# Kernel optimization log

Hardware: AMD Instinct MI355X
Metric: run time of the kernel (lower is better)

Reference implementation:

```python
import jax, jax.numpy as jnp
import numpy as np

GROUPS = 4

def shuffle(t):
    # torch Shuffle: transpose(-1,-2).contiguous().view(original_shape)
    return jnp.swapaxes(t, -1, -2).reshape(t.shape)

def setup_inputs() -> dict:
    key = jax.random.key(0)
    B, H = 131072, 512
    gh = 2 * H // GROUPS  # 256
    k = jax.random.split(key, 5)
    s = lambda fan_in: 1.0 / np.sqrt(fan_in)
    x = jax.random.normal(k[0], (B, H), dtype=jnp.float32)
    # weights stored as (in, out); Linear has bias=False throughout
    W1 = jax.random.uniform(k[1], (H, H), jnp.float32, -s(H), s(H))
    W2 = jax.random.uniform(k[2], (gh, gh), jnp.float32, -s(gh), s(gh))
    W3 = jax.random.uniform(k[3], (gh, gh), jnp.float32, -s(gh), s(gh))
    W4 = jax.random.uniform(k[4], (2 * H, H), jnp.float32, -s(2 * H), s(2 * H))
    return {"x": x, "W1": W1, "W2": W2, "W3": W3, "W4": W4}

def reference(x, W1, W2, W3, W4):
    B, H = x.shape
    gh = 2 * H // GROUPS
    sorted_x = jnp.sort(x, axis=1, stable=True)
    h = jnp.stack((x, sorted_x), axis=1)          # (B, 2, H)
    h = h @ W1                                    # (B, 2, H)
    h = h.reshape(B, GROUPS, gh)                  # Flatten + Unflatten
    h = shuffle(h)
    h = h @ W2                                    # (B, GROUPS, gh)
    h = shuffle(h)
    h = jax.nn.relu(h @ W3)                       # (B, GROUPS, gh)
    h = h.reshape(B, GROUPS * gh)                 # (B, 2H)
    scores = jax.nn.sigmoid(h @ W4)               # (B, H)
    return x * scores
```

## Files before the change

kernel.cpp:

```cpp
#include <hip/hip_runtime.h>
#include <hip/hip_bf16.h>
#include <cstdint>
#include <cstddef>

typedef short bf16x8 __attribute__((ext_vector_type(8)));
typedef float f32x4 __attribute__((ext_vector_type(4)));

#define BM 128
#define BN 128
#define BK 32

__device__ __forceinline__ void gl_lds16(const __hip_bfloat16* gp, __hip_bfloat16* lp) {
  __builtin_amdgcn_global_load_lds((const __attribute__((address_space(1))) void*)gp,
                                   (__attribute__((address_space(3))) void*)lp, 16, 0, 0);
}

__global__ void __launch_bounds__(256) wtrans_kernel(const float* __restrict__ src,
                                                     __hip_bfloat16* __restrict__ dst,
                                                     int R, int C) {
  int idx = blockIdx.x * 256 + threadIdx.x;
  if (idx >= R * C) return;
  int r = idx / C, c = idx % C;
  dst[(size_t)c * R + r] = __float2bfloat16(src[idx]);
}

__global__ void __launch_bounds__(256) sort_kernel(const float* __restrict__ x,
                                                   __hip_bfloat16* __restrict__ h0) {
  int row = blockIdx.x * 4 + (threadIdx.x >> 6);
  int lane = threadIdx.x & 63;
  const float* xr = x + (size_t)row * 512;

  float v[8];
  *(float4*)&v[0] = *(const float4*)&xr[lane * 8];
  *(float4*)&v[4] = *(const float4*)&xr[lane * 8 + 4];

  __hip_bfloat16* h = h0 + (size_t)row * 1024;
  {
    alignas(16) __hip_bfloat16 ob[8];
#pragma unroll
    for (int i = 0; i < 8; ++i) ob[i] = __float2bfloat16(v[i]);
    *(bf16x8*)&h[lane * 8] = *(const bf16x8*)ob;
  }

#pragma unroll
  for (int k = 2; k <= 512; k <<= 1) {
#pragma unroll
    for (int j = k >> 1; j > 0; j >>= 1) {
      if (j >= 8) {
        int L = j >> 3;
        bool lower = (lane & L) == 0;
        bool up = (((lane * 8) & k) == 0);
        bool sel = (lower == up);
#pragma unroll
        for (int r = 0; r < 8; ++r) {
          float pv = __shfl_xor(v[r], L, 64);
          float mn = fminf(v[r], pv), mx = fmaxf(v[r], pv);
          v[r] = sel ? mn : mx;
        }
      } else {
#pragma unroll
        for (int r = 0; r < 8; ++r) {
          if ((r & j) == 0) {
            int r2 = r | j;
            bool up = ((((lane * 8) + r) & k) == 0);
            float a = v[r], b = v[r2];
            float mn = fminf(a, b), mx = fmaxf(a, b);
            v[r] = up ? mn : mx;
            v[r2] = up ? mx : mn;
          }
        }
      }
    }
  }

  {
    alignas(16) __hip_bfloat16 ob[8];
#pragma unroll
    for (int i = 0; i < 8; ++i) ob[i] = __float2bfloat16(v[i]);
    *(bf16x8*)&h[512 + lane * 8] = *(const bf16x8*)ob;
  }
}

template <int EPI>
__global__ void __launch_bounds__(256) gemm_k(const __hip_bfloat16* __restrict__ A,
                                              const __hip_bfloat16* __restrict__ BT,
                                              __hip_bfloat16* __restrict__ Cb,
                                              float* __restrict__ Co,
                                              const float* __restrict__ X,
                                              int M, int N, int K) {
  __shared__ __hip_bfloat16 lA[BM * BK];
  __shared__ __hip_bfloat16 lB[BN * BK];

  int nwg = gridDim.x;
  int bid = blockIdx.x;
  int cpx = nwg >> 3;
  int wg = (bid & 7) * cpx + (bid >> 3);

  int nt = N / BN;
  int m0 = (wg / nt) * BM;
  int n0 = (wg % nt) * BN;

  int tid = threadIdx.x;
  int lane = tid & 63;
  int w = tid >> 6;
  int wm = (w >> 1) << 6;
  int wn = (w & 1) << 6;
  int r16 = lane & 15;
  int k8 = (lane >> 4) << 3;

  int colA = (lane & 3) * 8;
  int rsub = lane >> 2;
  int row0 = w * 16 + rsub;
  int row1 = (4 + w) * 16 + rsub;

  f32x4 acc[4][4] = {};

  for (int k0 = 0; k0 < K; k0 += BK) {
    gl_lds16(&A[(size_t)(m0 + row0) * K + k0 + colA], &lA[(size_t)w * 512]);
    gl_lds16(&A[(size_t)(m0 + row1) * K + k0 + colA], &lA[(size_t)(4 + w) * 512]);
    gl_lds16(&BT[(size_t)(n0 + row0) * K + k0 + colA], &lB[(size_t)w * 512]);
    gl_lds16(&BT[(size_t)(n0 + row1) * K + k0 + colA], &lB[(size_t)(4 + w) * 512]);
    asm volatile("s_waitcnt vmcnt(0)" ::: "memory");
    __syncthreads();

    bf16x8 af[4], bfr[4];
#pragma unroll
    for (int i = 0; i < 4; ++i)
      af[i] = *(const bf16x8*)&lA[(wm + 16 * i + r16) * BK + k8];
#pragma unroll
    for (int j = 0; j < 4; ++j)
      bfr[j] = *(const bf16x8*)&lB[(wn + 16 * j + r16) * BK + k8];
#pragma unroll
    for (int i = 0; i < 4; ++i)
#pragma unroll
      for (int j = 0; j < 4; ++j)
        acc[i][j] = __builtin_amdgcn_mfma_f32_16x16x32_bf16(af[i], bfr[j], acc[i][j], 0, 0, 0);
    __syncthreads();
  }

#pragma unroll
  for (int i = 0; i < 4; ++i) {
    int grow_base = m0 + wm + 16 * i + ((lane >> 4) << 2);
#pragma unroll
    for (int j = 0; j < 4; ++j) {
      int gcol = n0 + wn + 16 * j + (lane & 15);
#pragma unroll
      for (int r = 0; r < 4; ++r) {
        int grow = grow_base + r;
        float v = acc[i][j][r];
        if constexpr (EPI == 1) {
          int b = grow >> 1, p = grow & 1;
          Cb[(size_t)b * 1024 + 4 * (gcol & 255) + (p << 1) + (gcol >> 8)] = __float2bfloat16(v);
        } else if constexpr (EPI == 2) {
          int b = grow >> 2, g = grow & 3;
          Cb[(size_t)b * 1024 + 4 * gcol + g] = __float2bfloat16(v);
        } else if constexpr (EPI == 3) {
          Cb[(size_t)grow * N + gcol] = __float2bfloat16(fmaxf(v, 0.f));
        } else {
          float xv = X[(size_t)grow * N + gcol];
          Co[(size_t)grow * N + gcol] = xv / (1.f + __expf(-v));
        }
      }
    }
  }
}

extern "C" void kernel_launch(void* const* d_in, const int* in_sizes, int n_in,
                              void* d_out, int out_size, void* d_ws, size_t ws_size,
                              hipStream_t stream) {
  const float* x  = (const float*)d_in[0];
  const float* W1 = (const float*)d_in[1];
  const float* W2 = (const float*)d_in[2];
  const float* W3 = (const float*)d_in[3];
  const float* W4 = (const float*)d_in[4];

  const int B = 131072;

  char* ws = (char*)d_ws;
  __hip_bfloat16* W1T = (__hip_bfloat16*)(ws);
  __hip_bfloat16* W2T = (__hip_bfloat16*)(ws + 524288);
  __hip_bfloat16* W3T = (__hip_bfloat16*)(ws + 655360);
  __hip_bfloat16* W4T = (__hip_bfloat16*)(ws + 786432);
  __hip_bfloat16* bufA = (__hip_bfloat16*)(ws + 2097152);
  __hip_bfloat16* bufB = bufA + (size_t)134217728;

  wtrans_kernel<<<(512 * 512) / 256, 256, 0, stream>>>(W1, W1T, 512, 512);
  wtrans_kernel<<<(256 * 256) / 256, 256, 0, stream>>>(W2, W2T, 256, 256);
  wtrans_kernel<<<(256 * 256) / 256, 256, 0, stream>>>(W3, W3T, 256, 256);
  wtrans_kernel<<<(1024 * 512) / 256, 256, 0, stream>>>(W4, W4T, 1024, 512);

  sort_kernel<<<B / 4, 256, 0, stream>>>(x, bufA);

  gemm_k<1><<<(2 * B / BM) * (512 / BN), 256, 0, stream>>>(bufA, W1T, bufB, nullptr, nullptr,
                                                           2 * B, 512, 512);
  gemm_k<2><<<(4 * B / BM) * (256 / BN), 256, 0, stream>>>(bufB, W2T, bufA, nullptr, nullptr,
                                                           4 * B, 256, 256);
  gemm_k<3><<<(4 * B / BM) * (256 / BN), 256, 0, stream>>>(bufA, W3T, bufB, nullptr, nullptr,
                                                           4 * B, 256, 256);
  gemm_k<4><<<(B / BM) * (512 / BN), 256, 0, stream>>>(bufB, W4T, nullptr, (float*)d_out, x,
                                                       B, 512, 1024);
}
```

Measured before the change: 1.145 ms.

## Triple-buffer LDS tiles in GEMM to overlap global loads with MFMA

Replaces the single-buffered load-wait-compute loop with a three-stage LDS ring buffer. Tiles for step t+2 are prefetched via global_load_lds while MFMAs run on step t. Partial vmcnt waits plus one barrier per iteration replace the full drain and two syncthreads. LDS use triples to 48KB per block, which may lower occupancy. Ordering now relies on the vmcnt counts and a single s_barrier being correct.

```diff
diff --git a/kernel.cpp b/kernel.cpp
--- a/kernel.cpp
+++ b/kernel.cpp
@@ -9,6 +9,7 @@
 #define BM 128
 #define BN 128
 #define BK 32
+#define NBUF 3
 
 __device__ __forceinline__ void gl_lds16(const __hip_bfloat16* gp, __hip_bfloat16* lp) {
   __builtin_amdgcn_global_load_lds((const __attribute__((address_space(1))) void*)gp,
@@ -88,17 +89,17 @@
                                               float* __restrict__ Co,
                                               const float* __restrict__ X,
                                               int M, int N, int K) {
-  __shared__ __hip_bfloat16 lA[BM * BK];
-  __shared__ __hip_bfloat16 lB[BN * BK];
+  __shared__ __hip_bfloat16 lA[NBUF][BM * BK];
+  __shared__ __hip_bfloat16 lB[NBUF][BN * BK];
 
   int nwg = gridDim.x;
   int bid = blockIdx.x;
   int cpx = nwg >> 3;
   int wg = (bid & 7) * cpx + (bid >> 3);
 
-  int nt = N / BN;
-  int m0 = (wg / nt) * BM;
-  int n0 = (wg % nt) * BN;
+  int nt_tiles = N / BN;
+  int m0 = (wg / nt_tiles) * BM;
+  int n0 = (wg % nt_tiles) * BN;
 
   int tid = threadIdx.x;
   int lane = tid & 63;
@@ -115,28 +116,48 @@
 
   f32x4 acc[4][4] = {};
 
-  for (int k0 = 0; k0 < K; k0 += BK) {
-    gl_lds16(&A[(size_t)(m0 + row0) * K + k0 + colA], &lA[(size_t)w * 512]);
-    gl_lds16(&A[(size_t)(m0 + row1) * K + k0 + colA], &lA[(size_t)(4 + w) * 512]);
-    gl_lds16(&BT[(size_t)(n0 + row0) * K + k0 + colA], &lB[(size_t)w * 512]);
-    gl_lds16(&BT[(size_t)(n0 + row1) * K + k0 + colA], &lB[(size_t)(4 + w) * 512]);
-    asm volatile("s_waitcnt vmcnt(0)" ::: "memory");
-    __syncthreads();
+#define STAGE(t, buf)                                                          \
+  do {                                                                         \
+    int k0_ = (t) * BK;                                                        \
+    gl_lds16(&A[(size_t)(m0 + row0) * K + k0_ + colA], &lA[buf][w * 512]);     \
+    gl_lds16(&A[(size_t)(m0 + row1) * K + k0_ + colA], &lA[buf][(4 + w) * 512]); \
+    gl_lds16(&BT[(size_t)(n0 + row0) * K + k0_ + colA], &lB[buf][w * 512]);    \
+    gl_lds16(&BT[(size_t)(n0 + row1) * K + k0_ + colA], &lB[buf][(4 + w) * 512]); \
+  } while (0)
+
+  int nt = K / BK;
+  STAGE(0, 0);
+  STAGE(1, 1);
+  asm volatile("s_waitcnt vmcnt(4)" ::: "memory");
+  __builtin_amdgcn_s_barrier();
+
+  int cur = 0;
+  for (int t = 0; t < nt; ++t) {
+    int nb = cur + 2; if (nb >= NBUF) nb -= NBUF;
+    if (t + 2 < nt) STAGE(t + 2, nb);
 
     bf16x8 af[4], bfr[4];
 #pragma unroll
     for (int i = 0; i < 4; ++i)
-      af[i] = *(const bf16x8*)&lA[(wm + 16 * i + r16) * BK + k8];
+      af[i] = *(const bf16x8*)&lA[cur][(wm + 16 * i + r16) * BK + k8];
 #pragma unroll
     for (int j = 0; j < 4; ++j)
-      bfr[j] = *(const bf16x8*)&lB[(wn + 16 * j + r16) * BK + k8];
+      bfr[j] = *(const bf16x8*)&lB[cur][(wn + 16 * j + r16) * BK + k8];
 #pragma unroll
     for (int i = 0; i < 4; ++i)
 #pragma unroll
       for (int j = 0; j < 4; ++j)
         acc[i][j] = __builtin_amdgcn_mfma_f32_16x16x32_bf16(af[i], bfr[j], acc[i][j], 0, 0, 0);
-    __syncthreads();
-  }
+
+    if (t + 2 < nt) {
+      asm volatile("s_waitcnt vmcnt(4)" ::: "memory");
+    } else if (t + 1 < nt) {
+      asm volatile("s_waitcnt vmcnt(0)" ::: "memory");
+    }
+    if (t + 1 < nt) __builtin_amdgcn_s_barrier();
+    cur = (cur + 1 == NBUF) ? 0 : cur + 1;
+  }
+#undef STAGE
 
 #pragma unroll
   for (int i = 0; i < 4; ++i) {
```

Result: faster. 1.119 ms (-2.3%).

## Triple-buffer GEMM with larger tiles, XOR-swizzled LDS and 8 waves

Applied to the files above, without the earlier changes.

Reworks the GEMM kernel to use 256x128x64 tiles with 512 threads, a three-stage LDS ring that prefetches two K-steps ahead, and XOR-swizzled LDS layout to avoid bank conflicts. N and K become template parameters so the K loop fully unrolls, and s_setprio brackets the MFMA bursts. The aim is to overlap global-to-LDS loads with compute and cut barrier stalls and LDS conflicts. The cost is more LDS per block (about 144KB), which limits occupancy to one block per CU.

```diff
diff --git a/kernel.cpp b/kernel.cpp
--- a/kernel.cpp
+++ b/kernel.cpp
@@ -6,9 +6,9 @@
 typedef short bf16x8 __attribute__((ext_vector_type(8)));
 typedef float f32x4 __attribute__((ext_vector_type(4)));
 
-#define BM 128
+#define BM 256
 #define BN 128
-#define BK 32
+#define BK 64
 
 __device__ __forceinline__ void gl_lds16(const __hip_bfloat16* gp, __hip_bfloat16* lp) {
   __builtin_amdgcn_global_load_lds((const __attribute__((address_space(1))) void*)gp,
@@ -81,69 +81,114 @@
   }
 }
 
-template <int EPI>
-__global__ void __launch_bounds__(256) gemm_k(const __hip_bfloat16* __restrict__ A,
+template <int EPI, int N, int K>
+__global__ void __launch_bounds__(512) gemm_k(const __hip_bfloat16* __restrict__ A,
                                               const __hip_bfloat16* __restrict__ BT,
                                               __hip_bfloat16* __restrict__ Cb,
                                               float* __restrict__ Co,
-                                              const float* __restrict__ X,
-                                              int M, int N, int K) {
-  __shared__ __hip_bfloat16 lA[BM * BK];
-  __shared__ __hip_bfloat16 lB[BN * BK];
+                                              const float* __restrict__ X) {
+  __shared__ __hip_bfloat16 lA[3][BM * BK];
+  __shared__ __hip_bfloat16 lB[3][BN * BK];
 
   int nwg = gridDim.x;
   int bid = blockIdx.x;
   int cpx = nwg >> 3;
   int wg = (bid & 7) * cpx + (bid >> 3);
 
-  int nt = N / BN;
-  int m0 = (wg / nt) * BM;
-  int n0 = (wg % nt) * BN;
+  constexpr int NTN = N / BN;
+  int m0 = (wg / NTN) * BM;
+  int n0 = (wg % NTN) * BN;
 
   int tid = threadIdx.x;
   int lane = tid & 63;
   int w = tid >> 6;
-  int wm = (w >> 1) << 6;
-  int wn = (w & 1) << 6;
+  int wr = w >> 1;
+  int wc = w & 1;
   int r16 = lane & 15;
-  int k8 = (lane >> 4) << 3;
-
-  int colA = (lane & 3) * 8;
-  int rsub = lane >> 2;
-  int row0 = w * 16 + rsub;
-  int row1 = (4 + w) * 16 + rsub;
+  int g4 = lane >> 4;
+
+  int ar = lane >> 3;
+  int acs = 8 * ((lane & 7) ^ (ar & 7));
+  const __hip_bfloat16* Asrc = A + (size_t)(m0 + w * 32 + ar) * K + acs;
+  const __hip_bfloat16* Bsrc = BT + (size_t)(n0 + w * 16 + ar) * K + acs;
+
+  int xorr = (r16 & 7) * 8;
+  int arow[4], brow[4];
+#pragma unroll
+  for (int i = 0; i < 4; ++i) arow[i] = (wr * 64 + 16 * i + r16) * BK;
+#pragma unroll
+  for (int j = 0; j < 4; ++j) brow[j] = (wc * 64 + 16 * j + r16) * BK;
+  int kx0 = (g4 * 8) ^ xorr;
+  int kx1 = (32 + g4 * 8) ^ xorr;
 
   f32x4 acc[4][4] = {};
 
-  for (int k0 = 0; k0 < K; k0 += BK) {
-    gl_lds16(&A[(size_t)(m0 + row0) * K + k0 + colA], &lA[(size_t)w * 512]);
-    gl_lds16(&A[(size_t)(m0 + row1) * K + k0 + colA], &lA[(size_t)(4 + w) * 512]);
-    gl_lds16(&BT[(size_t)(n0 + row0) * K + k0 + colA], &lB[(size_t)w * 512]);
-    gl_lds16(&BT[(size_t)(n0 + row1) * K + k0 + colA], &lB[(size_t)(4 + w) * 512]);
-    asm volatile("s_waitcnt vmcnt(0)" ::: "memory");
-    __syncthreads();
-
-    bf16x8 af[4], bfr[4];
+#define STAGE(tt, bb)                                                     \
+  do {                                                                    \
+    int k0_ = (tt) * BK;                                                  \
+    gl_lds16(Asrc + k0_, &lA[bb][(w * 4 + 0) * 512]);                     \
+    gl_lds16(Asrc + (size_t)8 * K + k0_, &lA[bb][(w * 4 + 1) * 512]);     \
+    gl_lds16(Asrc + (size_t)16 * K + k0_, &lA[bb][(w * 4 + 2) * 512]);    \
+    gl_lds16(Asrc + (size_t)24 * K + k0_, &lA[bb][(w * 4 + 3) * 512]);    \
+    gl_lds16(Bsrc + k0_, &lB[bb][(w * 2 + 0) * 512]);                     \
+    gl_lds16(Bsrc + (size_t)8 * K + k0_, &lB[bb][(w * 2 + 1) * 512]);     \
+  } while (0)
+
+  constexpr int NT = K / BK;
+  STAGE(0, 0);
+  STAGE(1, 1);
+  asm volatile("s_waitcnt vmcnt(6)" ::: "memory");
+  __builtin_amdgcn_s_barrier();
+
+#pragma unroll
+  for (int t = 0; t < NT; ++t) {
+    const int cur = t % 3;
+    const int nxt = (t + 2) % 3;
+
+    bf16x8 a0[4], b0[4];
+#pragma unroll
+    for (int i = 0; i < 4; ++i) a0[i] = *(const bf16x8*)&lA[cur][arow[i] + kx0];
+#pragma unroll
+    for (int j = 0; j < 4; ++j) b0[j] = *(const bf16x8*)&lB[cur][brow[j] + kx0];
+
+    if (t + 2 < NT) STAGE(t + 2, nxt);
+
+    __builtin_amdgcn_s_setprio(1);
 #pragma unroll
     for (int i = 0; i < 4; ++i)
-      af[i] = *(const bf16x8*)&lA[(wm + 16 * i + r16) * BK + k8];
-#pragma unroll
-    for (int j = 0; j < 4; ++j)
-      bfr[j] = *(const bf16x8*)&lB[(wn + 16 * j + r16) * BK + k8];
+#pragma unroll
+      for (int j = 0; j < 4; ++j)
+        acc[i][j] = __builtin_amdgcn_mfma_f32_16x16x32_bf16(a0[i], b0[j], acc[i][j], 0, 0, 0);
+    __builtin_amdgcn_s_setprio(0);
+
+    bf16x8 a1[4], b1[4];
+#pragma unroll
+    for (int i = 0; i < 4; ++i) a1[i] = *(const bf16x8*)&lA[cur][arow[i] + kx1];
+#pragma unroll
+    for (int j = 0; j < 4; ++j) b1[j] = *(const bf16x8*)&lB[cur][brow[j] + kx1];
+
+    __builtin_amdgcn_s_setprio(1);
 #pragma unroll
     for (int i = 0; i < 4; ++i)
 #pragma unroll
       for (int j = 0; j < 4; ++j)
-        acc[i][j] = __builtin_amdgcn_mfma_f32_16x16x32_bf16(af[i], bfr[j], acc[i][j], 0, 0, 0);
-    __syncthreads();
-  }
+        acc[i][j] = __builtin_amdgcn_mfma_f32_16x16x32_bf16(a1[i], b1[j], acc[i][j], 0, 0, 0);
+    __builtin_amdgcn_s_setprio(0);
+
+    if (t + 1 < NT) {
+      if (t + 2 < NT) asm volatile("s_waitcnt vmcnt(6)" ::: "memory");
+      else            asm volatile("s_waitcnt vmcnt(0)" ::: "memory");
+      __builtin_amdgcn_s_barrier();
+    }
+  }
+#undef STAGE
 
 #pragma unroll
   for (int i = 0; i < 4; ++i) {
-    int grow_base = m0 + wm + 16 * i + ((lane >> 4) << 2);
+    int grow_base = m0 + wr * 64 + 16 * i + g4 * 4;
 #pragma unroll
     for (int j = 0; j < 4; ++j) {
-      int gcol = n0 + wn + 16 * j + (lane & 15);
+      int gcol = n0 + wc * 64 + 16 * j + r16;
 #pragma unroll
       for (int r = 0; r < 4; ++r) {
         int grow = grow_base + r;
@@ -191,12 +236,8 @@
 
   sort_kernel<<<B / 4, 256, 0, stream>>>(x, bufA);
 
-  gemm_k<1><<<(2 * B / BM) * (512 / BN), 256, 0, stream>>>(bufA, W1T, bufB, nullptr, nullptr,
-                                                           2 * B, 512, 512);
-  gemm_k<2><<<(4 * B / BM) * (256 / BN), 256, 0, stream>>>(bufB, W2T, bufA, nullptr, nullptr,
-                                                           4 * B, 256, 256);
-  gemm_k<3><<<(4 * B / BM) * (256 / BN), 256, 0, stream>>>(bufA, W3T, bufB, nullptr, nullptr,
-                                                           4 * B, 256, 256);
-  gemm_k<4><<<(B / BM) * (512 / BN), 256, 0, stream>>>(bufB, W4T, nullptr, (float*)d_out, x,
-                                                       B, 512, 1024);
-}
+  gemm_k<1, 512, 512><<<(2 * B / BM) * (512 / BN), 512, 0, stream>>>(bufA, W1T, bufB, nullptr, nullptr);
+  gemm_k<2, 256, 256><<<(4 * B / BM) * (256 / BN), 512, 0, stream>>>(bufB, W2T, bufA, nullptr, nullptr);
+  gemm_k<3, 256, 256><<<(4 * B / BM) * (256 / BN), 512, 0, stream>>>(bufA, W3T, bufB, nullptr, nullptr);
+  gemm_k<4, 512, 1024><<<(B / BM) * (512 / BN), 512, 0, stream>>>(bufB, W4T, nullptr, (float*)d_out, x);
+}
```

After: 1.108 ms. -3.2%, faster.
